# Kernel optimization log

Hardware: AMD Instinct MI355X
Metric: run time of the kernel (lower is better)

Reference implementation:

```python
import jax, jax.numpy as jnp
import numpy as np

EPS = 1e-5
D, C, T, H = 512, 256, 2, 2  # d_model, d_ctx, tokens, heads
HD = D // H                   # head dim


def _ln(x, g, b):
    m = x.mean(-1, keepdims=True)
    v = ((x - m) ** 2).mean(-1, keepdims=True)
    return (x - m) / jnp.sqrt(v + EPS) * g + b


def setup_inputs() -> dict:
    key = jax.random.key(0)
    ks = jax.random.split(key, 16)
    B, L = 8, 4096
    w = lambda k, s: (jax.random.normal(k, s, jnp.float32) * 0.02)
    Hc, H2 = 512, 1024  # ctx-head hidden = max(D,C); mix hidden = 2*D
    return {
        "x": jax.random.normal(ks[0], (B, L, D), jnp.float32),
        "context": jax.random.normal(ks[1], (B, C), jnp.float32),
        "pad_valid_mask": jax.random.bernoulli(ks[2], 0.9, (B, L)),
        "film_ln_g": jnp.ones(D), "film_ln_b": jnp.zeros(D),
        "film_w": w(ks[3], (2 * D, C)), "film_b": jnp.zeros(2 * D),
        "concat_w": w(ks[4], (D, D + C)), "concat_b": jnp.zeros(D),
        "concat_ln_g": jnp.ones(D), "concat_ln_b": jnp.zeros(D),
        "ctx_w1": w(ks[5], (Hc, C)), "ctx_b1": jnp.zeros(Hc),
        "ctx_w2": w(ks[6], (T * D, Hc)), "ctx_b2": jnp.zeros(T * D),
        "q_ln_g": jnp.ones(D), "q_ln_b": jnp.zeros(D),
        "in_proj_w": w(ks[7], (3 * D, D)), "in_proj_b": jnp.zeros(3 * D),
        "out_proj_w": w(ks[8], (D, D)), "out_proj_b": jnp.zeros(D),
        "mix_w1": w(ks[9], (H2, 4 * D)), "mix_b1": jnp.zeros(H2),
        "mix_w2": w(ks[10], (D, H2)), "mix_b2": jnp.zeros(D),
        "out_ln_g": jnp.ones(D), "out_ln_b": jnp.zeros(D),
        "gate_w": w(ks[11], (D, C)), "gate_b": jnp.zeros(D),
    }


def reference(x, context, pad_valid_mask,
              film_ln_g, film_ln_b, film_w, film_b,
              concat_w, concat_b, concat_ln_g, concat_ln_b,
              ctx_w1, ctx_b1, ctx_w2, ctx_b2,
              q_ln_g, q_ln_b, in_proj_w, in_proj_b, out_proj_w, out_proj_b,
              mix_w1, mix_b1, mix_w2, mix_b2,
              out_ln_g, out_ln_b, gate_w, gate_b):
    B, L, _ = x.shape
    film_gain, alpha_max = 1.0, 1.0
    # 1) HyperFiLM: base = (1 + gain*gamma) * LN(x) + gain*beta
    gb = context @ film_w.T + film_b                      # [B, 2D]
    gamma, beta = gb[:, :D], gb[:, D:]
    base = (1.0 + film_gain * gamma)[:, None, :] * _ln(x, film_ln_g, film_ln_b) \
           + (film_gain * beta)[:, None, :]
    # 2) Concat path
    ctx_exp = jnp.broadcast_to(context[:, None, :], (B, L, C))
    z = jnp.concatenate([x, ctx_exp], axis=-1)            # [B, L, D+C]
    upd_c = _ln(jax.nn.relu(z @ concat_w.T + concat_b), concat_ln_g, concat_ln_b)
    # 3) Cross-attn path: context -> T tokens
    h = jax.nn.gelu(context @ ctx_w1.T + ctx_b1, approximate=False)
    ctx_tok = (h @ ctx_w2.T + ctx_b2).reshape(B, T, D)
    x_q = _ln(x, q_ln_g, q_ln_b)
    wq, wk, wv = in_proj_w[:D], in_proj_w[D:2 * D], in_proj_w[2 * D:]
    bq, bk, bv = in_proj_b[:D], in_proj_b[D:2 * D], in_proj_b[2 * D:]
    q = (x_q @ wq.T + bq).reshape(B, L, H, HD)
    k = (ctx_tok @ wk.T + bk).reshape(B, T, H, HD)
    v = (ctx_tok @ wv.T + bv).reshape(B, T, H, HD)
    scores = jnp.einsum('blhd,bthd->bhlt', q, k) / jnp.sqrt(jnp.float32(HD))
    attn = jax.nn.softmax(scores, axis=-1)
    a = jnp.einsum('bhlt,bthd->blhd', attn, v).reshape(B, L, D)
    attn_out = a @ out_proj_w.T + out_proj_b
    mix_in = jnp.concatenate([x, attn_out, x - attn_out, x * attn_out], axis=-1)
    upd_a = jax.nn.relu(mix_in @ mix_w1.T + mix_b1) @ mix_w2.T + mix_b2
    # 4) Combine with sigmoid gate, alpha, pad mask
    gate = jax.nn.sigmoid(context @ gate_w.T + gate_b) * alpha_max  # [B, D]
    gate = gate[:, None, :] * pad_valid_mask[:, :, None].astype(x.dtype)
    out = _ln(base + gate * (upd_c + upd_a), out_ln_g, out_ln_b)
    return out
```

## Files before the change

### kernel.cpp

```cpp
#include <hip/hip_runtime.h>
#include <hip/hip_bf16.h>


#define N_TOK 32768
#define HALF_ROWS 16384

typedef unsigned short u16;
typedef __attribute__((ext_vector_type(8))) __bf16 bf16x8;
typedef __attribute__((ext_vector_type(4))) float f32x4;

__device__ __forceinline__ float bf2f(unsigned int h) { return __uint_as_float(h << 16); }
__device__ __forceinline__ u16 f2bf(float f) {
    unsigned int u = __float_as_uint(f);
    u += 0x7FFFu + ((u >> 16) & 1u);
    return (u16)(u >> 16);
}
__device__ __forceinline__ void load8(const u16* p, float* v) {
    uint4 u = *(const uint4*)p;
    v[0] = bf2f(u.x & 0xffffu); v[1] = bf2f(u.x >> 16);
    v[2] = bf2f(u.y & 0xffffu); v[3] = bf2f(u.y >> 16);
    v[4] = bf2f(u.z & 0xffffu); v[5] = bf2f(u.z >> 16);
    v[6] = bf2f(u.w & 0xffffu); v[7] = bf2f(u.w >> 16);
}
__device__ __forceinline__ uint4 pack8(const float* v) {
    uint4 u;
    u.x = (unsigned)f2bf(v[0]) | ((unsigned)f2bf(v[1]) << 16);
    u.y = (unsigned)f2bf(v[2]) | ((unsigned)f2bf(v[3]) << 16);
    u.z = (unsigned)f2bf(v[4]) | ((unsigned)f2bf(v[5]) << 16);
    u.w = (unsigned)f2bf(v[6]) | ((unsigned)f2bf(v[7]) << 16);
    return u;
}
__device__ __forceinline__ void async16(const u16* g, u16* lds) {
    __builtin_amdgcn_global_load_lds(
        (const __attribute__((address_space(1))) unsigned int*)g,
        (__attribute__((address_space(3))) unsigned int*)lds, 16, 0, 0);
}

#define FENCE() asm volatile("" ::: "memory")
#define BARRIER() do { FENCE(); __builtin_amdgcn_s_barrier(); FENCE(); } while (0)
#define WAITV(n) asm volatile("s_waitcnt vmcnt(" #n ")" ::: "memory")
#define LGKM0()  asm volatile("s_waitcnt lgkmcnt(0)" ::: "memory")

__global__ void prep_kernel(const float* __restrict__ in_proj_w,
                            const float* __restrict__ in_proj_b,
                            const float* __restrict__ qb,
                            const float* __restrict__ concat_w,
                            const float* __restrict__ mix_w1,
                            const float* __restrict__ mix_w2,
                            const float* __restrict__ context,
                            float* __restrict__ bqp,
                            u16* __restrict__ cwbf, u16* __restrict__ m1bf,
                            u16* __restrict__ m2bf, u16* __restrict__ ctxbf) {
    const int bid = blockIdx.x;
    const int tid = threadIdx.x;
    if (bid < 128) {
        const int wave = tid >> 6, lane = tid & 63;
        const int j = bid * 4 + wave;
        const int i = lane * 8;
        float4 w0 = *(const float4*)(in_proj_w + (size_t)j * 512 + i);
        float4 w1 = *(const float4*)(in_proj_w + (size_t)j * 512 + i + 4);
        float4 b0 = *(const float4*)(qb + i);
        float4 b1 = *(const float4*)(qb + i + 4);
        float p1 = w0.x*b0.x + w0.y*b0.y + w0.z*b0.z + w0.w*b0.w
                 + w1.x*b1.x + w1.y*b1.y + w1.z*b1.z + w1.w*b1.w;
        for (int m = 1; m < 64; m <<= 1) p1 += __shfl_xor(p1, m, 64);
        if (lane == 0) bqp[j] = in_proj_b[j] + p1;
    } else if (bid < 320) {
        int i = (bid - 128) * 256 + tid;
        const float* s = concat_w + (size_t)i * 8;
        float4 a = *(const float4*)s;
        float4 b = *(const float4*)(s + 4);
        float v[8] = {a.x, a.y, a.z, a.w, b.x, b.y, b.z, b.w};
        *(uint4*)(cwbf + (size_t)i * 8) = pack8(v);
    } else if (bid < 576) {
        int i = (bid - 320) * 256 + tid;
        const float* s = mix_w2 + (size_t)i * 8;
        float4 a = *(const float4*)s;
        float4 b = *(const float4*)(s + 4);
        float v[8] = {a.x, a.y, a.z, a.w, b.x, b.y, b.z, b.w};
        *(uint4*)(m2bf + (size_t)i * 8) = pack8(v);
    } else if (bid < 1344) {
        int idx = (bid - 576) * 256 + tid;
        int n = idx / 192;
        int k = (idx - n * 192) * 8;
        const float* base = mix_w1 + (size_t)n * 2048;
        float v[8];
        if (k < 512) {
            #pragma unroll
            for (int e = 0; e < 8; e++) v[e] = base[k + e] + base[1024 + k + e];
        } else if (k < 1024) {
            #pragma unroll
            for (int e = 0; e < 8; e++) v[e] = base[k + e] - base[512 + k + e];
        } else {
            #pragma unroll
            for (int e = 0; e < 8; e++) v[e] = base[512 + k + e];
        }
        *(uint4*)(m1bf + (size_t)n * 1536 + k) = pack8(v);
    } else {
        for (int i = tid; i < 2048; i += 256)
            ctxbf[i] = f2bf(context[i]);
    }
}

__global__ void ctx_stage_a(const float* __restrict__ context,
                            const float* __restrict__ film_w, const float* __restrict__ film_b,
                            const float* __restrict__ gate_w, const float* __restrict__ gate_b,
                            const float* __restrict__ ctx_w1, const float* __restrict__ ctx_b1,
                            float* __restrict__ gb1, float* __restrict__ betab,
                            float* __restrict__ gateb, float* __restrict__ hbuf) {
    const int wave = threadIdx.x >> 6, lane = threadIdx.x & 63;
    const int widx = blockIdx.x * 4 + wave;
    const int b   = widx >> 11;
    const int j2  = widx & 2047;
    const int cat = j2 >> 9;
    const int j   = j2 & 511;
    const float* wrow;
    if      (cat == 0) wrow = film_w + (size_t)j * 256;
    else if (cat == 1) wrow = film_w + (size_t)(512 + j) * 256;
    else if (cat == 2) wrow = gate_w + (size_t)j * 256;
    else               wrow = ctx_w1 + (size_t)j * 256;
    float4 wv = *(const float4*)(wrow + lane * 4);
    float4 cv = *(const float4*)(context + b * 256 + lane * 4);
    float s = wv.x * cv.x + wv.y * cv.y + wv.z * cv.z + wv.w * cv.w;
    for (int m = 1; m < 64; m <<= 1) s += __shfl_xor(s, m, 64);
    if (lane == 0) {
        if      (cat == 0) gb1[b * 512 + j]   = 1.0f + s + film_b[j];
        else if (cat == 1) betab[b * 512 + j] = s + film_b[512 + j];
        else if (cat == 2) gateb[b * 512 + j] = 1.f / (1.f + expf(-(s + gate_b[j])));
        else {
            float hv = s + ctx_b1[j];
            hbuf[b * 512 + j] = 0.5f * hv * (1.0f + erff(hv * 0.70710678118654752f));
        }
    }
}

__global__ void ctx_stage_b(const float* __restrict__ hbuf,
                            const float* __restrict__ ctx_w2, const float* __restrict__ ctx_b2,
                            float* __restrict__ tokbuf) {
    const int wave = threadIdx.x >> 6, lane = threadIdx.x & 63;
    const int widx = blockIdx.x * 4 + wave;
    const int b = widx >> 10;
    const int j = widx & 1023;
    const float* wrow = ctx_w2 + (size_t)j * 512 + lane * 8;
    const float* hr   = hbuf + b * 512 + lane * 8;
    float4 w0 = *(const float4*)wrow, w1 = *(const float4*)(wrow + 4);
    float4 h0 = *(const float4*)hr,   h1 = *(const float4*)(hr + 4);
    float s = w0.x*h0.x + w0.y*h0.y + w0.z*h0.z + w0.w*h0.w
            + w1.x*h1.x + w1.y*h1.y + w1.z*h1.z + w1.w*h1.w;
    for (int m = 1; m < 64; m <<= 1) s += __shfl_xor(s, m, 64);
    if (lane == 0) tokbuf[b * 1024 + j] = s + ctx_b2[j];
}

__global__ void ctx_stage_c(const float* __restrict__ tokbuf,
                            const float* __restrict__ in_proj_w, const float* __restrict__ in_proj_b,
                            float* __restrict__ kbuf, float* __restrict__ vbuf) {
    const int wave = threadIdx.x >> 6, lane = threadIdx.x & 63;
    const int widx = blockIdx.x * 4 + wave;
    const int b  = widx >> 11;
    const int r  = widx & 2047;
    const int t  = r >> 10;
    const int kv = (r >> 9) & 1;
    const int j  = r & 511;
    const float* wrow = in_proj_w + (size_t)(512 + kv * 512 + j) * 512 + lane * 8;
    const float* tk   = tokbuf + (b * 2 + t) * 512 + lane * 8;
    float4 w0 = *(const float4*)wrow, w1 = *(const float4*)(wrow + 4);
    float4 t0 = *(const float4*)tk,   t1 = *(const float4*)(tk + 4);
    float s = w0.x*t0.x + w0.y*t0.y + w0.z*t0.z + w0.w*t0.w
            + w1.x*t1.x + w1.y*t1.y + w1.z*t1.z + w1.w*t1.w;
    for (int m = 1; m < 64; m <<= 1) s += __shfl_xor(s, m, 64);
    if (lane == 0) {
        float v = s + in_proj_b[512 + kv * 512 + j];
        if (kv == 0) kbuf[(b * 2 + t) * 512 + j] = v;
        else         vbuf[(b * 2 + t) * 512 + j] = v;
    }
}

__global__ void ctx_stage_d(const float* __restrict__ in_proj_w,
                            const float* __restrict__ out_proj_w,
                            const float* __restrict__ qg, const float* __restrict__ bqp,
                            const float* __restrict__ kbuf, const float* __restrict__ vbuf,
                            float* __restrict__ ubuf, float* __restrict__ vobuf,
                            float* __restrict__ subuf, float* __restrict__ c0buf) {
    const int tid = threadIdx.x;
    __shared__ float sh[256];
    __shared__ float red[256];
    if (blockIdx.x < 32) {
        const int bid = blockIdx.x;
        const int b = bid >> 2, idx = bid & 3;
        const int t = idx >> 1, h = idx & 1;
        sh[tid] = kbuf[(b * 2 + t) * 512 + h * 256 + tid];
        __syncthreads();
        float a0 = 0.f, a1 = 0.f;
        #pragma unroll 4
        for (int dd = 0; dd < 256; dd++) {
            const float kv = sh[dd];
            const float* wr = in_proj_w + (size_t)(h * 256 + dd) * 512;
            a0 += kv * wr[tid];
            a1 += kv * wr[tid + 256];
        }
        float u0 = a0 * qg[tid], u1 = a1 * qg[tid + 256];
        ubuf[bid * 512 + tid]       = u0;
        ubuf[bid * 512 + tid + 256] = u1;
        red[tid] = u0 + u1;
        __syncthreads();
        for (int s = 128; s > 0; s >>= 1) { if (tid < s) red[tid] += red[tid + s]; __syncthreads(); }
        if (tid == 0) subuf[bid] = red[0];
        __syncthreads();
        red[tid] = bqp[h * 256 + tid] * sh[tid];
        __syncthreads();
        for (int s = 128; s > 0; s >>= 1) { if (tid < s) red[tid] += red[tid + s]; __syncthreads(); }
        if (tid == 0) c0buf[bid] = red[0];
    } else {
        const int bid = blockIdx.x - 32;
        const int b = bid >> 2, idx = bid & 3;
        const int t = idx >> 1, h = idx & 1;
        sh[tid] = vbuf[(b * 2 + t) * 512 + h * 256 + tid];
        __syncthreads();
        const float* w0 = out_proj_w + (size_t)tid * 512 + h * 256;
        const float* w1 = out_proj_w + (size_t)(tid + 256) * 512 + h * 256;
        float acc0 = 0.f, acc1 = 0.f;
        #pragma unroll 2
        for (int dd = 0; dd < 256; dd += 4) {
            float4 x0 = *(const float4*)(w0 + dd);
            float4 x1 = *(const float4*)(w1 + dd);
            acc0 += x0.x*sh[dd] + x0.y*sh[dd+1] + x0.z*sh[dd+2] + x0.w*sh[dd+3];
            acc1 += x1.x*sh[dd] + x1.y*sh[dd+1] + x1.z*sh[dd+2] + x1.w*sh[dd+3];
        }
        vobuf[bid * 512 + tid]       = acc0;
        vobuf[bid * 512 + tid + 256] = acc1;
    }
}

__global__ void statsattn_kernel(const float* __restrict__ x, float* __restrict__ stats,
                                 u16* __restrict__ mixA, u16* __restrict__ pbufH,
                                 const float* __restrict__ ubuf, const float* __restrict__ subuf,
                                 const float* __restrict__ c0buf, const float* __restrict__ vobuf,
                                 const float* __restrict__ ob, const int rowbase) {
    const int wave = threadIdx.x >> 6, lane = threadIdx.x & 63;
    const size_t lr = (size_t)blockIdx.x * 8 + wave * 2;
    const size_t gr = lr + rowbase;
    const int b = (int)(gr >> 12);
    float v[2][8], s[2] = {0.f, 0.f}, ss[2] = {0.f, 0.f};
    #pragma unroll
    for (int r = 0; r < 2; r++) {
        const float* xr = x + (gr + r) * 512 + lane * 8;
        float4 a = *(const float4*)xr;
        float4 c = *(const float4*)(xr + 4);
        v[r][0]=a.x; v[r][1]=a.y; v[r][2]=a.z; v[r][3]=a.w;
        v[r][4]=c.x; v[r][5]=c.y; v[r][6]=c.z; v[r][7]=c.w;
        #pragma unroll
        for (int e = 0; e < 8; e++) { s[r] += v[r][e]; ss[r] += v[r][e] * v[r][e]; }
    }
    float u[4][8];
    #pragma unroll
    for (int idx = 0; idx < 4; idx++) {
        const float* up = ubuf + (b * 4 + idx) * 512 + lane * 8;
        float4 u0 = *(const float4*)up, u1 = *(const float4*)(up + 4);
        u[idx][0]=u0.x; u[idx][1]=u0.y; u[idx][2]=u0.z; u[idx][3]=u0.w;
        u[idx][4]=u1.x; u[idx][5]=u1.y; u[idx][6]=u1.z; u[idx][7]=u1.w;
    }
    float sd[2][4];
    #pragma unroll
    for (int r = 0; r < 2; r++)
        #pragma unroll
        for (int idx = 0; idx < 4; idx++) {
            float acc = 0.f;
            #pragma unroll
            for (int e = 0; e < 8; e++) acc += v[r][e] * u[idx][e];
            sd[r][idx] = acc;
        }
    for (int m = 1; m < 64; m <<= 1) {
        #pragma unroll
        for (int r = 0; r < 2; r++) {
            s[r] += __shfl_xor(s[r], m, 64); ss[r] += __shfl_xor(ss[r], m, 64);
            #pragma unroll
            for (int idx = 0; idx < 4; idx++) sd[r][idx] += __shfl_xor(sd[r][idx], m, 64);
        }
    }
    float vo[4][8];
    #pragma unroll
    for (int idx = 0; idx < 4; idx++) {
        const float* vp = vobuf + (b * 4 + idx) * 512 + lane * 8;
        float4 v0 = *(const float4*)vp, v1 = *(const float4*)(vp + 4);
        vo[idx][0]=v0.x; vo[idx][1]=v0.y; vo[idx][2]=v0.z; vo[idx][3]=v0.w;
        vo[idx][4]=v1.x; vo[idx][5]=v1.y; vo[idx][6]=v1.z; vo[idx][7]=v1.w;
    }
    float obp[8];
    {
        const float* op = ob + lane * 8;
        float4 o0 = *(const float4*)op, o1 = *(const float4*)(op + 4);
        obp[0]=o0.x; obp[1]=o0.y; obp[2]=o0.z; obp[3]=o0.w;
        obp[4]=o1.x; obp[5]=o1.y; obp[6]=o1.z; obp[7]=o1.w;
    }
    #pragma unroll
    for (int r = 0; r < 2; r++) {
        const float mean = s[r] * (1.f / 512.f);
        const float rstd = rsqrtf(ss[r] * (1.f / 512.f) - mean * mean + 1e-5f);
        if (lane == 0) { stats[(gr + r) * 2] = mean; stats[(gr + r) * 2 + 1] = rstd; }
        float sc[4];
        #pragma unroll
        for (int idx = 0; idx < 4; idx++)
            sc[idx] = (rstd * (sd[r][idx] - mean * subuf[b * 4 + idx]) + c0buf[b * 4 + idx]) * (1.f / 16.f);
        float p[4];
        #pragma unroll
        for (int h = 0; h < 2; h++) {
            float s0 = sc[h], s1 = sc[2 + h];
            float mx = fmaxf(s0, s1);
            float e0 = expf(s0 - mx), e1 = expf(s1 - mx);
            float inv = 1.f / (e0 + e1);
            p[h] = e0 * inv; p[2 + h] = e1 * inv;
        }
        float o[8], pr[8];
        #pragma unroll
        for (int e = 0; e < 8; e++) {
            o[e] = p[0]*vo[0][e] + p[1]*vo[1][e] + p[2]*vo[2][e] + p[3]*vo[3][e] + obp[e];
            pr[e] = v[r][e] * o[e];
        }
        *(uint4*)(mixA + (gr + r) * 1024 + lane * 8)       = pack8(v[r]);
        *(uint4*)(mixA + (gr + r) * 1024 + 512 + lane * 8) = pack8(o);
        *(uint4*)(pbufH + (lr + r) * 512 + lane * 8)       = pack8(pr);
    }
}

template<int AMODE, int NT, bool RELU>
__launch_bounds__(512, 2)
__global__ void mix_gemm8(const u16* __restrict__ A0, const u16* __restrict__ A1,
                          const u16* __restrict__ Wb, const float* __restrict__ bias,
                          u16* __restrict__ out, const int ldo) {
    constexpr int BLD = NT * 64;
    constexpr int NIT = NT / 2;
    extern __shared__ __align__(16) u16 S[];
    u16* As = S;
    u16* Bs = S + 32768;
    const int tid = threadIdx.x;
    const int l = tid & 63;
    const int w = tid >> 6;
    const int wm = w >> 2, wn = w & 3;
    const int quad = l >> 4, lc = l & 15;
    const size_t m0 = (size_t)blockIdx.x * 256;
    const int n0 = blockIdx.y * 256;
    const int bidx = (int)(m0 >> 12);

    const int r0 = tid >> 3;
    const int r1 = (tid + 512) >> 3;
    const int c0s = ((tid & 7) ^ (r0 & 7)) * 8;
    const int c1s = ((tid & 7) ^ (r1 & 7)) * 8;

    auto stA = [&](int kt, int h, int buf) {
        u16* dst = As + (buf * 2 + h) * 8192;
        if constexpr (AMODE == 0) {
            async16(A0 + (m0 + h * 128 + r0) * 1024 + kt * 64 + c0s, dst + tid * 8);
            async16(A0 + (m0 + h * 128 + r1) * 1024 + kt * 64 + c1s, dst + (tid + 512) * 8);
        } else if constexpr (AMODE == 1) {
            if (kt < 8) {
                async16(A0 + (m0 + h * 128 + r0) * 1024 + kt * 64 + c0s, dst + tid * 8);
                async16(A0 + (m0 + h * 128 + r1) * 1024 + kt * 64 + c1s, dst + (tid + 512) * 8);
            } else {
                async16(A1 + bidx * 256 + (kt - 8) * 64 + c0s, dst + tid * 8);
                async16(A1 + bidx * 256 + (kt - 8) * 64 + c1s, dst + (tid + 512) * 8);
            }
        } else {
            if (kt < 16) {
                async16(A0 + (m0 + h * 128 + r0) * 1024 + kt * 64 + c0s, dst + tid * 8);
                async16(A0 + (m0 + h * 128 + r1) * 1024 + kt * 64 + c1s, dst + (tid + 512) * 8);
            } else {
                async16(A1 + (m0 + h * 128 + r0) * 512 + (kt - 16) * 64 + c0s, dst + tid * 8);
                async16(A1 + (m0 + h * 128 + r1) * 512 + (kt - 16) * 64 + c1s, dst + (tid + 512) * 8);
            }
        }
    };
    auto stB = [&](int kt, int h, int buf) {
        u16* dst = Bs + (buf * 2 + h) * 8192;
        async16(Wb + (size_t)(n0 + h * 128 + r0) * BLD + kt * 64 + c0s, dst + tid * 8);
        async16(Wb + (size_t)(n0 + h * 128 + r1) * BLD + kt * 64 + c1s, dst + (tid + 512) * 8);
    };

    bf16x8 a_[4][2], b_[2][2][2];
    f32x4 acc[8][4];
    #pragma unroll
    for (int i = 0; i < 8; i++)
        #pragma unroll
        for (int j = 0; j < 4; j++) acc[i][j] = (f32x4){0.f, 0.f, 0.f, 0.f};

    auto rdA = [&](int buf, int qi) {
        const u16* Ab = As + (buf * 2 + wm) * 8192;
        #pragma unroll
        for (int ii = 0; ii < 4; ii++) {
            const int r = (qi * 4 + ii) * 16 + lc;
            #pragma unroll
            for (int kk = 0; kk < 2; kk++) {
                const int cs = (kk * 4 + quad) ^ (r & 7);
                a_[ii][kk] = *(const bf16x8*)&Ab[r * 64 + cs * 8];
            }
        }
    };
    auto rdB = [&](int buf, int qj) {
        #pragma unroll
        for (int jj = 0; jj < 2; jj++) {
            const int nr = wn * 64 + (qj * 2 + jj) * 16 + lc;
            const int hb = nr >> 7, r = nr & 127;
            const u16* Bb = Bs + (buf * 2 + hb) * 8192;
            #pragma unroll
            for (int kk = 0; kk < 2; kk++) {
                const int cs = (kk * 4 + quad) ^ (r & 7);
                b_[qj][jj][kk] = *(const bf16x8*)&Bb[r * 64 + cs * 8];
            }
        }
    };
    auto mfma16 = [&](int qi, int qj) {
        __builtin_amdgcn_s_setprio(1);
        #pragma unroll
        for (int ii = 0; ii < 4; ii++)
            #pragma unroll
            for (int jj = 0; jj < 2; jj++)
                #pragma unroll
                for (int kk = 0; kk < 2; kk++)
                    acc[qi * 4 + ii][qj * 2 + jj] = __builtin_amdgcn_mfma_f32_16x16x32_bf16(
                        a_[ii][kk], b_[qj][jj][kk], acc[qi * 4 + ii][qj * 2 + jj], 0, 0, 0);
        __builtin_amdgcn_s_setprio(0);
    };

    stA(0, 0, 0); stA(0, 1, 0); stB(0, 0, 0); stB(0, 1, 0);
    stA(1, 0, 1);
    WAITV(2); BARRIER();

    for (int it = 0; it < NIT; it++) {
        const int tb = 2 * it + 1;
        const bool more = (it < NIT - 1);
        rdA(0, 0); rdB(0, 0);
        stA(tb, 1, 1);
        BARRIER(); mfma16(0, 0);
        rdB(0, 1);
        stB(tb, 0, 1);
        BARRIER(); mfma16(0, 1);
        rdA(0, 1);
        stB(tb, 1, 1);
        BARRIER(); mfma16(1, 1);
        BARRIER();
        if (more) { stA(tb + 1, 0, 0); WAITV(2); }
        else      { WAITV(0); }
        BARRIER(); mfma16(1, 0);
        rdA(1, 0); rdB(1, 0);
        if (more) stA(tb + 1, 1, 0);
        BARRIER(); mfma16(0, 0);
        rdB(1, 1);
        if (more) stB(tb + 1, 0, 0);
        BARRIER(); mfma16(0, 1);
        rdA(1, 1);
        if (more) stB(tb + 1, 1, 0);
        BARRIER(); mfma16(1, 1);
        BARRIER();
        if (more) { stA(tb + 2, 0, 1); WAITV(2); }
        BARRIER(); mfma16(1, 0);
    }

    BARRIER();
    float bv[4];
    #pragma unroll
    for (int j = 0; j < 4; j++) bv[j] = bias[n0 + wn * 64 + j * 16 + lc];
    #pragma unroll
    for (int p = 0; p < 2; p++) {
        if (p) BARRIER();
        if (wm == p) {
            #pragma unroll
            for (int i = 0; i < 8; i++)
                #pragma unroll
                for (int j = 0; j < 4; j++)
                    #pragma unroll
                    for (int reg = 0; reg < 4; reg++) {
                        float vv = acc[i][j][reg] + bv[j];
                        if (RELU) vv = fmaxf(vv, 0.f);
                        S[(i * 16 + quad * 4 + reg) * 264 + wn * 64 + j * 16 + lc] = f2bf(vv);
                    }
        }
        LGKM0(); BARRIER();
        #pragma unroll
        for (int kq = 0; kq < 8; kq++) {
            const int cix = tid + kq * 512;
            const int row = cix >> 5, ch = cix & 31;
            *(uint4*)(out + (m0 + p * 128 + row) * (size_t)ldo + n0 + ch * 8)
                = *(const uint4*)&S[row * 264 + ch * 8];
        }
    }
}

__global__ void final_kernel(const u16* __restrict__ mixA, const float* __restrict__ stats,
                             const u16* __restrict__ bufc,
                             const float* __restrict__ cg, const float* __restrict__ cb,
                             const float* __restrict__ gb1, const float* __restrict__ betab,
                             const float* __restrict__ gateb, const int* __restrict__ mask,
                             const float* __restrict__ fg, const float* __restrict__ fb,
                             const float* __restrict__ og, const float* __restrict__ ob,
                             float* __restrict__ out) {
    const int wave = threadIdx.x >> 6, lane = threadIdx.x & 63;
    const size_t row = (size_t)blockIdx.x * 4 + wave;
    const int b = (int)(row >> 12);
    const int c0 = lane * 8;
    float xv[8], uc[8], ua[8];
    load8(mixA + row * 1024 + c0, xv);
    load8(mixA + row * 1024 + 512 + c0, ua);
    load8(bufc + row * 512 + c0, uc);
    float sc = 0.f, ssc = 0.f;
    #pragma unroll
    for (int e = 0; e < 8; e++) { sc += uc[e]; ssc += uc[e] * uc[e]; }
    for (int m = 1; m < 64; m <<= 1) { sc += __shfl_xor(sc, m, 64); ssc += __shfl_xor(ssc, m, 64); }
    const float mc = sc * (1.f / 512.f);
    const float rc = rsqrtf(ssc * (1.f / 512.f) - mc * mc + 1e-5f);
    const float mean = stats[row * 2], rstd = stats[row * 2 + 1];
    const float mf = (mask[row] != 0) ? 1.f : 0.f;
    float y[8];
    float s = 0.f, ss = 0.f;
    #pragma unroll
    for (int e = 0; e < 8; e++) {
        int c = c0 + e;
        float ucn = (uc[e] - mc) * rc * cg[c] + cb[c];
        float xh = (xv[e] - mean) * rstd;
        float base = gb1[b * 512 + c] * (xh * fg[c] + fb[c]) + betab[b * 512 + c];
        float yv = base + gateb[b * 512 + c] * mf * (ucn + ua[e]);
        y[e] = yv; s += yv; ss += yv * yv;
    }
    for (int m = 1; m < 64; m <<= 1) { s += __shfl_xor(s, m, 64); ss += __shfl_xor(ss, m, 64); }
    float mean2 = s * (1.f / 512.f);
    float rstd2 = rsqrtf(ss * (1.f / 512.f) - mean2 * mean2 + 1e-5f);
    float o[8];
    #pragma unroll
    for (int e = 0; e < 8; e++) {
        int c = c0 + e;
        o[e] = (y[e] - mean2) * rstd2 * og[c] + ob[c];
    }
    *(float4*)(out + row * 512 + c0)     = make_float4(o[0], o[1], o[2], o[3]);
    *(float4*)(out + row * 512 + c0 + 4) = make_float4(o[4], o[5], o[6], o[7]);
}

extern "C" void kernel_launch(void* const* d_in, const int* in_sizes, int n_in,
                              void* d_out, int out_size, void* d_ws, size_t ws_size,
                              hipStream_t stream) {
    const float* x          = (const float*)d_in[0];
    const float* context    = (const float*)d_in[1];
    const int*   mask       = (const int*)d_in[2];
    const float* film_ln_g  = (const float*)d_in[3];
    const float* film_ln_b  = (const float*)d_in[4];
    const float* film_w     = (const float*)d_in[5];
    const float* film_b     = (const float*)d_in[6];
    const float* concat_w   = (const float*)d_in[7];
    const float* concat_b   = (const float*)d_in[8];
    const float* concat_ln_g= (const float*)d_in[9];
    const float* concat_ln_b= (const float*)d_in[10];
    const float* ctx_w1     = (const float*)d_in[11];
    const float* ctx_b1     = (const float*)d_in[12];
    const float* ctx_w2     = (const float*)d_in[13];
    const float* ctx_b2     = (const float*)d_in[14];
    const float* q_ln_g     = (const float*)d_in[15];
    const float* q_ln_b     = (const float*)d_in[16];
    const float* in_proj_w  = (const float*)d_in[17];
    const float* in_proj_b  = (const float*)d_in[18];
    const float* out_proj_w = (const float*)d_in[19];
    const float* out_proj_b = (const float*)d_in[20];
    const float* mix_w1     = (const float*)d_in[21];
    const float* mix_b1     = (const float*)d_in[22];
    const float* mix_w2     = (const float*)d_in[23];
    const float* mix_b2     = (const float*)d_in[24];
    const float* out_ln_g   = (const float*)d_in[25];
    const float* out_ln_b   = (const float*)d_in[26];
    const float* gate_w     = (const float*)d_in[27];
    const float* gate_b     = (const float*)d_in[28];
    float* out = (float*)d_out;

    float* gb1    = (float*)d_ws;
    float* betab  = gb1 + 4096;
    float* gateb  = betab + 4096;
    float* kbuf   = gateb + 4096;
    float* vbuf   = kbuf + 8192;
    float* bqp    = vbuf + 8192;
    float* hbuf   = bqp + 512;
    float* tokbuf = hbuf + 4096;
    float* ubuf   = tokbuf + 8192;
    float* vobuf  = ubuf + 16384;
    float* subuf  = vobuf + 16384;
    float* c0buf  = subuf + 32;
    float* stats  = c0buf + 32;
    u16* ctxbf = (u16*)(stats + 65536);
    u16* cwbf  = ctxbf + 2048;
    u16* m1bf  = cwbf + 393216;
    u16* m2bf  = m1bf + 1572864;
    u16* mixA  = m2bf + 524288;
    u16* bufh  = mixA + (size_t)N_TOK * 1024;
    u16* bufc  = bufh;
    u16* pbufH = bufh + (size_t)N_TOK * 1024;

    static bool attr_set = false;
    if (!attr_set) {
        hipFuncSetAttribute(reinterpret_cast<const void*>(&mix_gemm8<2, 24, true>),
                            hipFuncAttributeMaxDynamicSharedMemorySize, 131072);
        hipFuncSetAttribute(reinterpret_cast<const void*>(&mix_gemm8<0, 16, false>),
                            hipFuncAttributeMaxDynamicSharedMemorySize, 131072);
        hipFuncSetAttribute(reinterpret_cast<const void*>(&mix_gemm8<1, 12, true>),
                            hipFuncAttributeMaxDynamicSharedMemorySize, 131072);
        attr_set = true;
    }

    prep_kernel<<<1345, 256, 0, stream>>>(in_proj_w, in_proj_b, q_ln_b,
                                          concat_w, mix_w1, mix_w2, context,
                                          bqp, cwbf, m1bf, m2bf, ctxbf);
    ctx_stage_a<<<4096, 256, 0, stream>>>(context, film_w, film_b, gate_w, gate_b,
                                          ctx_w1, ctx_b1, gb1, betab, gateb, hbuf);
    ctx_stage_b<<<2048, 256, 0, stream>>>(hbuf, ctx_w2, ctx_b2, tokbuf);
    ctx_stage_c<<<4096, 256, 0, stream>>>(tokbuf, in_proj_w, in_proj_b, kbuf, vbuf);
    ctx_stage_d<<<64, 256, 0, stream>>>(in_proj_w, out_proj_w, q_ln_g, bqp,
                                        kbuf, vbuf, ubuf, vobuf, subuf, c0buf);

    for (int h = 0; h < 2; h++) {
        const int rowbase = h * HALF_ROWS;
        statsattn_kernel<<<HALF_ROWS / 8, 256, 0, stream>>>(
            x, stats, mixA, pbufH, ubuf, subuf, c0buf, vobuf, out_proj_b, rowbase);
        mix_gemm8<2, 24, true><<<dim3(64, 4), 512, 131072, stream>>>(
            mixA + (size_t)rowbase * 1024, pbufH, m1bf, mix_b1,
            bufh + (size_t)rowbase * 1024, 1024);
    }
    mix_gemm8<0, 16, false><<<dim3(128, 2), 512, 131072, stream>>>(
        bufh, nullptr, m2bf, mix_b2, mixA + 512, 1024);

    mix_gemm8<1, 12, true><<<dim3(128, 2), 512, 131072, stream>>>(
        mixA, ctxbf, cwbf, concat_b, bufc, 512);

    final_kernel<<<N_TOK / 4, 256, 0, stream>>>(mixA, stats, bufc,
                                                concat_ln_g, concat_ln_b,
                                                gb1, betab, gateb, mask,
                                                film_ln_g, film_ln_b,
                                                out_ln_g, out_ln_b, out);
    (void)in_sizes; (void)n_in; (void)out_size; (void)ws_size;
}
```

Measured before the change: 424.0 us.

## Fuse context-prep stages and first statsattn half into one cooperative kernel

Replaces the five small context-processing launches (prep, ctx stages a–d) and the first-half statsattn launch with one cooperative kernel that runs them in grid-stride loops separated by grid-wide syncs. The aim is to remove per-launch overhead and tail gaps between the many tiny dependent kernels that precede the mix GEMMs. In exchange it adds grid.sync barriers on a fixed 512-block grid, which may run each phase with less parallelism than the original launches, and it requires cooperative-launch residency.

Measured after the change: 833.4 us. 96.6% more time.

```diff
diff --git a/kernel.cpp b/kernel.cpp
--- a/kernel.cpp
+++ b/kernel.cpp
@@ -1,5 +1,8 @@
 #include <hip/hip_runtime.h>
 #include <hip/hip_bf16.h>
+#include <hip/hip_cooperative_groups.h>
+
+namespace cg = cooperative_groups;
 
 
 #define N_TOK 32768
@@ -41,18 +44,18 @@
 #define WAITV(n) asm volatile("s_waitcnt vmcnt(" #n ")" ::: "memory")
 #define LGKM0()  asm volatile("s_waitcnt lgkmcnt(0)" ::: "memory")
 
-__global__ void prep_kernel(const float* __restrict__ in_proj_w,
-                            const float* __restrict__ in_proj_b,
-                            const float* __restrict__ qb,
-                            const float* __restrict__ concat_w,
-                            const float* __restrict__ mix_w1,
-                            const float* __restrict__ mix_w2,
-                            const float* __restrict__ context,
-                            float* __restrict__ bqp,
-                            u16* __restrict__ cwbf, u16* __restrict__ m1bf,
-                            u16* __restrict__ m2bf, u16* __restrict__ ctxbf) {
-    const int bid = blockIdx.x;
-    const int tid = threadIdx.x;
+
+__device__ void prep_body(unsigned bid, int tid,
+                          const float* __restrict__ in_proj_w,
+                          const float* __restrict__ in_proj_b,
+                          const float* __restrict__ qb,
+                          const float* __restrict__ concat_w,
+                          const float* __restrict__ mix_w1,
+                          const float* __restrict__ mix_w2,
+                          const float* __restrict__ context,
+                          float* __restrict__ bqp,
+                          u16* __restrict__ cwbf, u16* __restrict__ m1bf,
+                          u16* __restrict__ m2bf, u16* __restrict__ ctxbf) {
     if (bid < 128) {
         const int wave = tid >> 6, lane = tid & 63;
         const int j = bid * 4 + wave;
@@ -102,14 +105,15 @@
     }
 }
 
-__global__ void ctx_stage_a(const float* __restrict__ context,
-                            const float* __restrict__ film_w, const float* __restrict__ film_b,
-                            const float* __restrict__ gate_w, const float* __restrict__ gate_b,
-                            const float* __restrict__ ctx_w1, const float* __restrict__ ctx_b1,
-                            float* __restrict__ gb1, float* __restrict__ betab,
-                            float* __restrict__ gateb, float* __restrict__ hbuf) {
-    const int wave = threadIdx.x >> 6, lane = threadIdx.x & 63;
-    const int widx = blockIdx.x * 4 + wave;
+__device__ void ctx_a_body(unsigned task, int tid,
+                           const float* __restrict__ context,
+                           const float* __restrict__ film_w, const float* __restrict__ film_b,
+                           const float* __restrict__ gate_w, const float* __restrict__ gate_b,
+                           const float* __restrict__ ctx_w1, const float* __restrict__ ctx_b1,
+                           float* __restrict__ gb1, float* __restrict__ betab,
+                           float* __restrict__ gateb, float* __restrict__ hbuf) {
+    const int wave = tid >> 6, lane = tid & 63;
+    const int widx = (int)task * 4 + wave;
     const int b   = widx >> 11;
     const int j2  = widx & 2047;
     const int cat = j2 >> 9;
@@ -134,11 +138,12 @@
     }
 }
 
-__global__ void ctx_stage_b(const float* __restrict__ hbuf,
-                            const float* __restrict__ ctx_w2, const float* __restrict__ ctx_b2,
-                            float* __restrict__ tokbuf) {
-    const int wave = threadIdx.x >> 6, lane = threadIdx.x & 63;
-    const int widx = blockIdx.x * 4 + wave;
+__device__ void ctx_b_body(unsigned task, int tid,
+                           const float* __restrict__ hbuf,
+                           const float* __restrict__ ctx_w2, const float* __restrict__ ctx_b2,
+                           float* __restrict__ tokbuf) {
+    const int wave = tid >> 6, lane = tid & 63;
+    const int widx = (int)task * 4 + wave;
     const int b = widx >> 10;
     const int j = widx & 1023;
     const float* wrow = ctx_w2 + (size_t)j * 512 + lane * 8;
@@ -151,11 +156,12 @@
     if (lane == 0) tokbuf[b * 1024 + j] = s + ctx_b2[j];
 }
 
-__global__ void ctx_stage_c(const float* __restrict__ tokbuf,
-                            const float* __restrict__ in_proj_w, const float* __restrict__ in_proj_b,
-                            float* __restrict__ kbuf, float* __restrict__ vbuf) {
-    const int wave = threadIdx.x >> 6, lane = threadIdx.x & 63;
-    const int widx = blockIdx.x * 4 + wave;
+__device__ void ctx_c_body(unsigned task, int tid,
+                           const float* __restrict__ tokbuf,
+                           const float* __restrict__ in_proj_w, const float* __restrict__ in_proj_b,
+                           float* __restrict__ kbuf, float* __restrict__ vbuf) {
+    const int wave = tid >> 6, lane = tid & 63;
+    const int widx = (int)task * 4 + wave;
     const int b  = widx >> 11;
     const int r  = widx & 2047;
     const int t  = r >> 10;
@@ -175,17 +181,15 @@
     }
 }
 
-__global__ void ctx_stage_d(const float* __restrict__ in_proj_w,
-                            const float* __restrict__ out_proj_w,
-                            const float* __restrict__ qg, const float* __restrict__ bqp,
-                            const float* __restrict__ kbuf, const float* __restrict__ vbuf,
-                            float* __restrict__ ubuf, float* __restrict__ vobuf,
-                            float* __restrict__ subuf, float* __restrict__ c0buf) {
-    const int tid = threadIdx.x;
-    __shared__ float sh[256];
-    __shared__ float red[256];
-    if (blockIdx.x < 32) {
-        const int bid = blockIdx.x;
+__device__ void ctx_d_body(unsigned task, int tid, float* sh, float* red,
+                           const float* __restrict__ in_proj_w,
+                           const float* __restrict__ out_proj_w,
+                           const float* __restrict__ qg, const float* __restrict__ bqp,
+                           const float* __restrict__ kbuf, const float* __restrict__ vbuf,
+                           float* __restrict__ ubuf, float* __restrict__ vobuf,
+                           float* __restrict__ subuf, float* __restrict__ c0buf) {
+    if (task < 32) {
+        const int bid = (int)task;
         const int b = bid >> 2, idx = bid & 3;
         const int t = idx >> 1, h = idx & 1;
         sh[tid] = kbuf[(b * 2 + t) * 512 + h * 256 + tid];
@@ -211,7 +215,7 @@
         for (int s = 128; s > 0; s >>= 1) { if (tid < s) red[tid] += red[tid + s]; __syncthreads(); }
         if (tid == 0) c0buf[bid] = red[0];
     } else {
-        const int bid = blockIdx.x - 32;
+        const int bid = (int)task - 32;
         const int b = bid >> 2, idx = bid & 3;
         const int t = idx >> 1, h = idx & 1;
         sh[tid] = vbuf[(b * 2 + t) * 512 + h * 256 + tid];
@@ -228,16 +232,18 @@
         }
         vobuf[bid * 512 + tid]       = acc0;
         vobuf[bid * 512 + tid + 256] = acc1;
-    }
-}
-
-__global__ void statsattn_kernel(const float* __restrict__ x, float* __restrict__ stats,
-                                 u16* __restrict__ mixA, u16* __restrict__ pbufH,
-                                 const float* __restrict__ ubuf, const float* __restrict__ subuf,
-                                 const float* __restrict__ c0buf, const float* __restrict__ vobuf,
-                                 const float* __restrict__ ob, const int rowbase) {
-    const int wave = threadIdx.x >> 6, lane = threadIdx.x & 63;
-    const size_t lr = (size_t)blockIdx.x * 8 + wave * 2;
+        __syncthreads();
+    }
+}
+
+__device__ void statsattn_body(unsigned task, int tid, int rowbase,
+                               const float* __restrict__ x, float* __restrict__ stats,
+                               u16* __restrict__ mixA, u16* __restrict__ pbufH,
+                               const float* __restrict__ ubuf, const float* __restrict__ subuf,
+                               const float* __restrict__ c0buf, const float* __restrict__ vobuf,
+                               const float* __restrict__ ob) {
+    const int wave = tid >> 6, lane = tid & 63;
+    const size_t lr = (size_t)task * 8 + wave * 2;
     const size_t gr = lr + rowbase;
     const int b = (int)(gr >> 12);
     float v[2][8], s[2] = {0.f, 0.f}, ss[2] = {0.f, 0.f};
@@ -320,6 +326,59 @@
         *(uint4*)(mixA + (gr + r) * 1024 + 512 + lane * 8) = pack8(o);
         *(uint4*)(pbufH + (lr + r) * 512 + lane * 8)       = pack8(pr);
     }
+}
+
+__launch_bounds__(256, 2)
+__global__ void ctx_fused(const float* in_proj_w, const float* in_proj_b, const float* qb,
+                          const float* concat_w, const float* mix_w1, const float* mix_w2,
+                          const float* context,
+                          float* bqp, u16* cwbf, u16* m1bf, u16* m2bf, u16* ctxbf,
+                          const float* film_w, const float* film_b,
+                          const float* gate_w, const float* gate_b,
+                          const float* ctx_w1, const float* ctx_b1,
+                          float* gb1, float* betab, float* gateb, float* hbuf,
+                          const float* ctx_w2, const float* ctx_b2, float* tokbuf,
+                          float* kbuf, float* vbuf,
+                          const float* out_proj_w, const float* qg,
+                          float* ubuf, float* vobuf, float* subuf, float* c0buf,
+                          const float* x, float* stats, u16* mixA, u16* pbufH,
+                          const float* ob) {
+    cg::grid_group grid = cg::this_grid();
+    const int tid = threadIdx.x;
+    __shared__ float sh[256];
+    __shared__ float red[256];
+
+    for (unsigned t = blockIdx.x; t < 5441u; t += gridDim.x) {
+        if (t < 1345u)
+            prep_body(t, tid, in_proj_w, in_proj_b, qb, concat_w, mix_w1, mix_w2,
+                      context, bqp, cwbf, m1bf, m2bf, ctxbf);
+        else
+            ctx_a_body(t - 1345u, tid, context, film_w, film_b, gate_w, gate_b,
+                       ctx_w1, ctx_b1, gb1, betab, gateb, hbuf);
+    }
+    __threadfence(); grid.sync();
+    for (unsigned t = blockIdx.x; t < 2048u; t += gridDim.x)
+        ctx_b_body(t, tid, hbuf, ctx_w2, ctx_b2, tokbuf);
+    __threadfence(); grid.sync();
+    for (unsigned t = blockIdx.x; t < 4096u; t += gridDim.x)
+        ctx_c_body(t, tid, tokbuf, in_proj_w, in_proj_b, kbuf, vbuf);
+    __threadfence(); grid.sync();
+    for (unsigned t = blockIdx.x; t < 64u; t += gridDim.x)
+        ctx_d_body(t, tid, sh, red, in_proj_w, out_proj_w, qg, bqp,
+                   kbuf, vbuf, ubuf, vobuf, subuf, c0buf);
+    __threadfence(); grid.sync();
+    for (unsigned t = blockIdx.x; t < 2048u; t += gridDim.x)
+        statsattn_body(t, tid, 0, x, stats, mixA, pbufH,
+                       ubuf, subuf, c0buf, vobuf, ob);
+}
+
+__global__ void statsattn_kernel(const float* __restrict__ x, float* __restrict__ stats,
+                                 u16* __restrict__ mixA, u16* __restrict__ pbufH,
+                                 const float* __restrict__ ubuf, const float* __restrict__ subuf,
+                                 const float* __restrict__ c0buf, const float* __restrict__ vobuf,
+                                 const float* __restrict__ ob, const int rowbase) {
+    statsattn_body(blockIdx.x, threadIdx.x, rowbase, x, stats, mixA, pbufH,
+                   ubuf, subuf, c0buf, vobuf, ob);
 }
 
 template<int AMODE, int NT, bool RELU>
@@ -486,7 +545,7 @@
 
 __global__ void final_kernel(const u16* __restrict__ mixA, const float* __restrict__ stats,
                              const u16* __restrict__ bufc,
-                             const float* __restrict__ cg, const float* __restrict__ cb,
+                             const float* __restrict__ cg_, const float* __restrict__ cb,
                              const float* __restrict__ gb1, const float* __restrict__ betab,
                              const float* __restrict__ gateb, const int* __restrict__ mask,
                              const float* __restrict__ fg, const float* __restrict__ fb,
@@ -513,7 +572,7 @@
     #pragma unroll
     for (int e = 0; e < 8; e++) {
         int c = c0 + e;
-        float ucn = (uc[e] - mc) * rc * cg[c] + cb[c];
+        float ucn = (uc[e] - mc) * rc * cg_[c] + cb[c];
         float xh = (xv[e] - mean) * rstd;
         float base = gb1[b * 512 + c] * (xh * fg[c] + fb[c]) + betab[b * 512 + c];
         float yv = base + gateb[b * 512 + c] * mf * (ucn + ua[e]);
@@ -599,24 +658,34 @@
         attr_set = true;
     }
 
-    prep_kernel<<<1345, 256, 0, stream>>>(in_proj_w, in_proj_b, q_ln_b,
-                                          concat_w, mix_w1, mix_w2, context,
-                                          bqp, cwbf, m1bf, m2bf, ctxbf);
-    ctx_stage_a<<<4096, 256, 0, stream>>>(context, film_w, film_b, gate_w, gate_b,
-                                          ctx_w1, ctx_b1, gb1, betab, gateb, hbuf);
-    ctx_stage_b<<<2048, 256, 0, stream>>>(hbuf, ctx_w2, ctx_b2, tokbuf);
-    ctx_stage_c<<<4096, 256, 0, stream>>>(tokbuf, in_proj_w, in_proj_b, kbuf, vbuf);
-    ctx_stage_d<<<64, 256, 0, stream>>>(in_proj_w, out_proj_w, q_ln_g, bqp,
-                                        kbuf, vbuf, ubuf, vobuf, subuf, c0buf);
-
-    for (int h = 0; h < 2; h++) {
-        const int rowbase = h * HALF_ROWS;
-        statsattn_kernel<<<HALF_ROWS / 8, 256, 0, stream>>>(
-            x, stats, mixA, pbufH, ubuf, subuf, c0buf, vobuf, out_proj_b, rowbase);
-        mix_gemm8<2, 24, true><<<dim3(64, 4), 512, 131072, stream>>>(
-            mixA + (size_t)rowbase * 1024, pbufH, m1bf, mix_b1,
-            bufh + (size_t)rowbase * 1024, 1024);
-    }
+    {
+        void* kargs[] = {
+            (void*)&in_proj_w, (void*)&in_proj_b, (void*)&q_ln_b,
+            (void*)&concat_w, (void*)&mix_w1, (void*)&mix_w2,
+            (void*)&context,
+            (void*)&bqp, (void*)&cwbf, (void*)&m1bf, (void*)&m2bf, (void*)&ctxbf,
+            (void*)&film_w, (void*)&film_b,
+            (void*)&gate_w, (void*)&gate_b,
+            (void*)&ctx_w1, (void*)&ctx_b1,
+            (void*)&gb1, (void*)&betab, (void*)&gateb, (void*)&hbuf,
+            (void*)&ctx_w2, (void*)&ctx_b2, (void*)&tokbuf,
+            (void*)&kbuf, (void*)&vbuf,
+            (void*)&out_proj_w, (void*)&q_ln_g,
+            (void*)&ubuf, (void*)&vobuf, (void*)&subuf, (void*)&c0buf,
+            (void*)&x, (void*)&stats, (void*)&mixA, (void*)&pbufH,
+            (void*)&out_proj_b };
+        hipLaunchCooperativeKernel(reinterpret_cast<const void*>(&ctx_fused),
+                                   dim3(512), dim3(256), kargs, 0, stream);
+    }
+
+    mix_gemm8<2, 24, true><<<dim3(64, 4), 512, 131072, stream>>>(
+        mixA, pbufH, m1bf, mix_b1, bufh, 1024);
+    statsattn_kernel<<<HALF_ROWS / 8, 256, 0, stream>>>(
+        x, stats, mixA, pbufH, ubuf, subuf, c0buf, vobuf, out_proj_b, HALF_ROWS);
+    mix_gemm8<2, 24, true><<<dim3(64, 4), 512, 131072, stream>>>(
+        mixA + (size_t)HALF_ROWS * 1024, pbufH, m1bf, mix_b1,
+        bufh + (size_t)HALF_ROWS * 1024, 1024);
+
     mix_gemm8<0, 16, false><<<dim3(128, 2), 512, 131072, stream>>>(
         bufh, nullptr, m2bf, mix_b2, mixA + 512, 1024);
 
```

## Merge prep and ctx stage A launches; reorder GEMM tile prefetch schedule

Applied to the files above, without the earlier changes.

Combines the weight-conversion prep kernel and the first context projection kernel into one launch, using the block index to pick the work, which removes one launch and its inter-kernel gap. It also reorders the double-buffered global-to-LDS prefetch in the mix GEMM main loop so that B tiles are staged ahead and A tiles follow in a different order, with extra barriers and different vmcnt waits. The schedule change alters how load latency overlaps MFMA work and adds barriers, which could cost as much as it saves.

Result: no change. 424.9 us (+0.2%).

```diff
diff --git a/kernel.cpp b/kernel.cpp
--- a/kernel.cpp
+++ b/kernel.cpp
@@ -41,18 +41,18 @@
 #define WAITV(n) asm volatile("s_waitcnt vmcnt(" #n ")" ::: "memory")
 #define LGKM0()  asm volatile("s_waitcnt lgkmcnt(0)" ::: "memory")
 
-__global__ void prep_kernel(const float* __restrict__ in_proj_w,
-                            const float* __restrict__ in_proj_b,
-                            const float* __restrict__ qb,
-                            const float* __restrict__ concat_w,
-                            const float* __restrict__ mix_w1,
-                            const float* __restrict__ mix_w2,
-                            const float* __restrict__ context,
-                            float* __restrict__ bqp,
-                            u16* __restrict__ cwbf, u16* __restrict__ m1bf,
-                            u16* __restrict__ m2bf, u16* __restrict__ ctxbf) {
-    const int bid = blockIdx.x;
-    const int tid = threadIdx.x;
+
+__device__ void prep_body(unsigned bid, int tid,
+                          const float* __restrict__ in_proj_w,
+                          const float* __restrict__ in_proj_b,
+                          const float* __restrict__ qb,
+                          const float* __restrict__ concat_w,
+                          const float* __restrict__ mix_w1,
+                          const float* __restrict__ mix_w2,
+                          const float* __restrict__ context,
+                          float* __restrict__ bqp,
+                          u16* __restrict__ cwbf, u16* __restrict__ m1bf,
+                          u16* __restrict__ m2bf, u16* __restrict__ ctxbf) {
     if (bid < 128) {
         const int wave = tid >> 6, lane = tid & 63;
         const int j = bid * 4 + wave;
@@ -102,14 +102,15 @@
     }
 }
 
-__global__ void ctx_stage_a(const float* __restrict__ context,
-                            const float* __restrict__ film_w, const float* __restrict__ film_b,
-                            const float* __restrict__ gate_w, const float* __restrict__ gate_b,
-                            const float* __restrict__ ctx_w1, const float* __restrict__ ctx_b1,
-                            float* __restrict__ gb1, float* __restrict__ betab,
-                            float* __restrict__ gateb, float* __restrict__ hbuf) {
-    const int wave = threadIdx.x >> 6, lane = threadIdx.x & 63;
-    const int widx = blockIdx.x * 4 + wave;
+__device__ void ctx_a_body(unsigned task, int tid,
+                           const float* __restrict__ context,
+                           const float* __restrict__ film_w, const float* __restrict__ film_b,
+                           const float* __restrict__ gate_w, const float* __restrict__ gate_b,
+                           const float* __restrict__ ctx_w1, const float* __restrict__ ctx_b1,
+                           float* __restrict__ gb1, float* __restrict__ betab,
+                           float* __restrict__ gateb, float* __restrict__ hbuf) {
+    const int wave = tid >> 6, lane = tid & 63;
+    const int widx = (int)task * 4 + wave;
     const int b   = widx >> 11;
     const int j2  = widx & 2047;
     const int cat = j2 >> 9;
@@ -132,6 +133,29 @@
             hbuf[b * 512 + j] = 0.5f * hv * (1.0f + erff(hv * 0.70710678118654752f));
         }
     }
+}
+
+__global__ void prep_ctxa_kernel(const float* __restrict__ in_proj_w,
+                                 const float* __restrict__ in_proj_b,
+                                 const float* __restrict__ qb,
+                                 const float* __restrict__ concat_w,
+                                 const float* __restrict__ mix_w1,
+                                 const float* __restrict__ mix_w2,
+                                 const float* __restrict__ context,
+                                 float* __restrict__ bqp,
+                                 u16* __restrict__ cwbf, u16* __restrict__ m1bf,
+                                 u16* __restrict__ m2bf, u16* __restrict__ ctxbf,
+                                 const float* __restrict__ film_w, const float* __restrict__ film_b,
+                                 const float* __restrict__ gate_w, const float* __restrict__ gate_b,
+                                 const float* __restrict__ ctx_w1, const float* __restrict__ ctx_b1,
+                                 float* __restrict__ gb1, float* __restrict__ betab,
+                                 float* __restrict__ gateb, float* __restrict__ hbuf) {
+    if (blockIdx.x < 1345)
+        prep_body(blockIdx.x, threadIdx.x, in_proj_w, in_proj_b, qb, concat_w,
+                  mix_w1, mix_w2, context, bqp, cwbf, m1bf, m2bf, ctxbf);
+    else
+        ctx_a_body(blockIdx.x - 1345, threadIdx.x, context, film_w, film_b,
+                   gate_w, gate_b, ctx_w1, ctx_b1, gb1, betab, gateb, hbuf);
 }
 
 __global__ void ctx_stage_b(const float* __restrict__ hbuf,
@@ -421,36 +445,36 @@
     };
 
     stA(0, 0, 0); stA(0, 1, 0); stB(0, 0, 0); stB(0, 1, 0);
-    stA(1, 0, 1);
-    WAITV(2); BARRIER();
+    stB(1, 0, 1); stB(1, 1, 1);
+    WAITV(4); BARRIER();
 
     for (int it = 0; it < NIT; it++) {
-        const int tb = 2 * it + 1;
-        const bool more = (it < NIT - 1);
+        const int t0 = 2 * it, t1 = 2 * it + 1;
+        const bool more = (it + 1 < NIT);
         rdA(0, 0); rdB(0, 0);
-        stA(tb, 1, 1);
+        stA(t1, 0, 1);
         BARRIER(); mfma16(0, 0);
         rdB(0, 1);
-        stB(tb, 0, 1);
+        stA(t1, 1, 1);
         BARRIER(); mfma16(0, 1);
+        BARRIER();
         rdA(0, 1);
-        stB(tb, 1, 1);
+        if (more) stB(t0 + 2, 0, 0);
         BARRIER(); mfma16(1, 1);
-        BARRIER();
-        if (more) { stA(tb + 1, 0, 0); WAITV(2); }
+        if (more) { stB(t0 + 2, 1, 0); WAITV(4); }
         else      { WAITV(0); }
         BARRIER(); mfma16(1, 0);
         rdA(1, 0); rdB(1, 0);
-        if (more) stA(tb + 1, 1, 0);
+        if (more) stA(t0 + 2, 0, 0);
         BARRIER(); mfma16(0, 0);
         rdB(1, 1);
-        if (more) stB(tb + 1, 0, 0);
+        if (more) stA(t0 + 2, 1, 0);
         BARRIER(); mfma16(0, 1);
+        BARRIER();
         rdA(1, 1);
-        if (more) stB(tb + 1, 1, 0);
+        if (more) stB(t1 + 2, 0, 1);
         BARRIER(); mfma16(1, 1);
-        BARRIER();
-        if (more) { stA(tb + 2, 0, 1); WAITV(2); }
+        if (more) { stB(t1 + 2, 1, 1); WAITV(4); }
         BARRIER(); mfma16(1, 0);
     }
 
@@ -486,7 +510,7 @@
 
 __global__ void final_kernel(const u16* __restrict__ mixA, const float* __restrict__ stats,
                              const u16* __restrict__ bufc,
-                             const float* __restrict__ cg, const float* __restrict__ cb,
+                             const float* __restrict__ cg_, const float* __restrict__ cb,
                              const float* __restrict__ gb1, const float* __restrict__ betab,
                              const float* __restrict__ gateb, const int* __restrict__ mask,
                              const float* __restrict__ fg, const float* __restrict__ fb,
@@ -513,7 +537,7 @@
     #pragma unroll
     for (int e = 0; e < 8; e++) {
         int c = c0 + e;
-        float ucn = (uc[e] - mc) * rc * cg[c] + cb[c];
+        float ucn = (uc[e] - mc) * rc * cg_[c] + cb[c];
         float xh = (xv[e] - mean) * rstd;
         float base = gb1[b * 512 + c] * (xh * fg[c] + fb[c]) + betab[b * 512 + c];
         float yv = base + gateb[b * 512 + c] * mf * (ucn + ua[e]);
@@ -599,11 +623,11 @@
         attr_set = true;
     }
 
-    prep_kernel<<<1345, 256, 0, stream>>>(in_proj_w, in_proj_b, q_ln_b,
-                                          concat_w, mix_w1, mix_w2, context,
-                                          bqp, cwbf, m1bf, m2bf, ctxbf);
-    ctx_stage_a<<<4096, 256, 0, stream>>>(context, film_w, film_b, gate_w, gate_b,
-                                          ctx_w1, ctx_b1, gb1, betab, gateb, hbuf);
+    prep_ctxa_kernel<<<5441, 256, 0, stream>>>(
+        in_proj_w, in_proj_b, q_ln_b, concat_w, mix_w1, mix_w2, context,
+        bqp, cwbf, m1bf, m2bf, ctxbf,
+        film_w, film_b, gate_w, gate_b, ctx_w1, ctx_b1,
+        gb1, betab, gateb, hbuf);
     ctx_stage_b<<<2048, 256, 0, stream>>>(hbuf, ctx_w2, ctx_b2, tokbuf);
     ctx_stage_c<<<4096, 256, 0, stream>>>(tokbuf, in_proj_w, in_proj_b, kbuf, vbuf);
     ctx_stage_d<<<64, 256, 0, stream>>>(in_proj_w, out_proj_w, q_ln_g, bqp,
```
